# Optimization experiments

Measured on AMD Instinct MI355X. Metric: run time of the kernel, lower is better.

## Reference

```python
import jax, jax.numpy as jnp
import numpy as np

N, E = 50000, 1600000
IN_DIM, EMBED, OUT = 512, 128, 64


def setup_inputs() -> dict:
    key = jax.random.key(0)
    k = jax.random.split(key, 8)
    x = jax.random.normal(k[0], (N, IN_DIM), dtype=jnp.float32)
    edge_index = jax.random.randint(k[1], (2, E), 0, N, dtype=jnp.int32)
    W_dense = jax.random.normal(k[2], (EMBED, IN_DIM), dtype=jnp.float32) * 0.02
    b_dense = jnp.zeros((EMBED,), dtype=jnp.float32)
    W_gat = jax.random.normal(k[3], (OUT, EMBED), dtype=jnp.float32) * 0.05
    att_src = jax.random.normal(k[4], (OUT,), dtype=jnp.float32) * 0.1
    att_dst = jax.random.normal(k[5], (OUT,), dtype=jnp.float32) * 0.1
    b_gat = jnp.zeros((OUT,), dtype=jnp.float32)
    return {"x": x, "edge_index": edge_index, "W_dense": W_dense, "b_dense": b_dense,
            "W_gat": W_gat, "att_src": att_src, "att_dst": att_dst, "b_gat": b_gat}


def reference(x, edge_index, W_dense, b_dense, W_gat, att_src, att_dst, b_gat):
    # dense -> LeakyReLU(0.01) (nn.LeakyReLU default)
    h = jax.nn.leaky_relu(x @ W_dense.T + b_dense, negative_slope=0.01)  # [N, EMBED]
    n = h.shape[0]
    # GATConv (PyG, heads=1, add_self_loops=True, negative_slope=0.2)
    loops = jnp.arange(n, dtype=edge_index.dtype)
    src = jnp.concatenate([edge_index[0], loops])
    dst = jnp.concatenate([edge_index[1], loops])
    g = h @ W_gat.T  # [N, OUT]
    a_src = g @ att_src  # [N]
    a_dst = g @ att_dst  # [N]
    e = jax.nn.leaky_relu(a_src[src] + a_dst[dst], negative_slope=0.2)  # [E+N]
    # segment softmax over destination neighborhoods (self loops guarantee non-empty)
    m = jax.ops.segment_max(e, dst, num_segments=n)
    e = jnp.exp(e - m[dst])
    denom = jax.ops.segment_sum(e, dst, num_segments=n)
    alpha = e / denom[dst]
    out = jax.ops.segment_sum(g[src] * alpha[:, None], dst, num_segments=n) + b_gat
    # original returns ([embed_x], [embed_x]); we return the single embedding tensor
    return out
```

## Files before the change

kernel.cpp:

```cpp
#include <hip/hip_runtime.h>
#include <math.h>

#define IN_DIM 512
#define EMBED 128
#define OUT_DIM 64

typedef __attribute__((ext_vector_type(8))) short bf16x8;
typedef __attribute__((ext_vector_type(4))) float f32x4;

__device__ __forceinline__ float lrelu(float v, float s) { return v > 0.f ? v : v * s; }

__device__ __forceinline__ float readlane_f(float v, int l) {
  return __int_as_float(__builtin_amdgcn_readlane(__float_as_int(v), l));
}

__device__ __forceinline__ unsigned short f2bf(float f) {
  unsigned int u = __float_as_uint(f);
  u += 0x7fff + ((u >> 16) & 1);
  return (unsigned short)(u >> 16);
}
__device__ __forceinline__ float bf2f(unsigned short h) {
  return __uint_as_float(((unsigned int)h) << 16);
}

#define LDA 40

__global__ __launch_bounds__(256) void gemm1_mfma_kernel(
    const float* __restrict__ x, const float* __restrict__ Wd,
    const float* __restrict__ bd, float* __restrict__ h, int N) {
  __shared__ __align__(16) unsigned short Ah[128][LDA];
  __shared__ __align__(16) unsigned short Al[128][LDA];
  __shared__ __align__(16) unsigned short Bh[64][LDA];
  __shared__ __align__(16) unsigned short Bl[64][LDA];

  const int tid = threadIdx.x;
  const int lane = tid & 63;
  const int wid = tid >> 6;
  const int wr = wid >> 1, wc = wid & 1;
  const int mblk = blockIdx.x * 128;
  const int nblk = blockIdx.y * 64;
  const int quad = lane >> 4;
  const int l15 = lane & 15;

  const int arow = tid >> 1, acb = (tid & 1) * 16;
  const int brow = tid >> 2, bcb = (tid & 3) * 8;
  const bool avalid = (mblk + arow) < N;
  const float* aptr = x + (size_t)(mblk + arow) * IN_DIM + acb;
  const float* bptr = Wd + (size_t)(nblk + brow) * IN_DIM + bcb;

  f32x4 acc[4][2];
#pragma unroll
  for (int i = 0; i < 4; ++i)
#pragma unroll
    for (int j = 0; j < 2; ++j) acc[i][j] = (f32x4){0.f, 0.f, 0.f, 0.f};

  for (int k0 = 0; k0 < IN_DIM; k0 += 32) {
    float4 t0, t1, t2, t3;
    if (avalid) {
      t0 = *(const float4*)(aptr + k0);
      t1 = *(const float4*)(aptr + k0 + 4);
      t2 = *(const float4*)(aptr + k0 + 8);
      t3 = *(const float4*)(aptr + k0 + 12);
    } else {
      t0 = t1 = t2 = t3 = make_float4(0.f, 0.f, 0.f, 0.f);
    }
    float4 u0 = *(const float4*)(bptr + k0);
    float4 u1 = *(const float4*)(bptr + k0 + 4);

    float av[16] = {t0.x, t0.y, t0.z, t0.w, t1.x, t1.y, t1.z, t1.w,
                    t2.x, t2.y, t2.z, t2.w, t3.x, t3.y, t3.z, t3.w};
    union { unsigned short us[16]; uint4 v[2]; } AH, AL;
#pragma unroll
    for (int i = 0; i < 16; ++i) {
      unsigned short hi = f2bf(av[i]);
      AH.us[i] = hi;
      AL.us[i] = f2bf(av[i] - bf2f(hi));
    }
    float bv[8] = {u0.x, u0.y, u0.z, u0.w, u1.x, u1.y, u1.z, u1.w};
    union { unsigned short us[8]; uint4 v; } BH, BL;
#pragma unroll
    for (int i = 0; i < 8; ++i) {
      unsigned short hi = f2bf(bv[i]);
      BH.us[i] = hi;
      BL.us[i] = f2bf(bv[i] - bf2f(hi));
    }

    __syncthreads();
    *(uint4*)&Ah[arow][acb] = AH.v[0];
    *(uint4*)&Ah[arow][acb + 8] = AH.v[1];
    *(uint4*)&Al[arow][acb] = AL.v[0];
    *(uint4*)&Al[arow][acb + 8] = AL.v[1];
    *(uint4*)&Bh[brow][bcb] = BH.v;
    *(uint4*)&Bl[brow][bcb] = BL.v;
    __syncthreads();

    bf16x8 ah[4], al[4], bh[2], bl[2];
#pragma unroll
    for (int mi = 0; mi < 4; ++mi) {
      int r = wr * 64 + mi * 16 + l15;
      ah[mi] = *(const bf16x8*)&Ah[r][quad * 8];
      al[mi] = *(const bf16x8*)&Al[r][quad * 8];
    }
#pragma unroll
    for (int ni = 0; ni < 2; ++ni) {
      int r = wc * 32 + ni * 16 + l15;
      bh[ni] = *(const bf16x8*)&Bh[r][quad * 8];
      bl[ni] = *(const bf16x8*)&Bl[r][quad * 8];
    }
#pragma unroll
    for (int mi = 0; mi < 4; ++mi)
#pragma unroll
      for (int ni = 0; ni < 2; ++ni) {
        acc[mi][ni] = __builtin_amdgcn_mfma_f32_16x16x32_bf16(ah[mi], bh[ni], acc[mi][ni], 0, 0, 0);
        acc[mi][ni] = __builtin_amdgcn_mfma_f32_16x16x32_bf16(al[mi], bh[ni], acc[mi][ni], 0, 0, 0);
        acc[mi][ni] = __builtin_amdgcn_mfma_f32_16x16x32_bf16(ah[mi], bl[ni], acc[mi][ni], 0, 0, 0);
      }
  }

#pragma unroll
  for (int mi = 0; mi < 4; ++mi)
#pragma unroll
    for (int ni = 0; ni < 2; ++ni) {
      int n = nblk + wc * 32 + ni * 16 + l15;
      float b = bd[n];
#pragma unroll
      for (int r = 0; r < 4; ++r) {
        int m = mblk + wr * 64 + mi * 16 + quad * 4 + r;
        if (m < N) h[(size_t)m * EMBED + n] = lrelu(acc[mi][ni][r] + b, 0.01f);
      }
    }
}

__global__ __launch_bounds__(256) void gemm2_mfma_kernel(
    const float* __restrict__ h, const float* __restrict__ Wg,
    const float* __restrict__ att_src, const float* __restrict__ att_dst,
    float* __restrict__ g, float* __restrict__ a_src, float* __restrict__ a_dst,
    int N) {
  __shared__ __align__(16) unsigned short Ah[128][LDA];
  __shared__ __align__(16) unsigned short Al[128][LDA];
  __shared__ __align__(16) unsigned short Bh[64][LDA];
  __shared__ __align__(16) unsigned short Bl[64][LDA];

  const int tid = threadIdx.x;
  const int lane = tid & 63;
  const int wid = tid >> 6;
  const int wr = wid >> 1, wc = wid & 1;
  const int mblk = blockIdx.x * 128;
  const int quad = lane >> 4;
  const int l15 = lane & 15;

  const int arow = tid >> 1, acb = (tid & 1) * 16;
  const int brow = tid >> 2, bcb = (tid & 3) * 8;
  const bool avalid = (mblk + arow) < N;
  const float* aptr = h + (size_t)(mblk + arow) * EMBED + acb;
  const float* bptr = Wg + (size_t)brow * EMBED + bcb;

  f32x4 acc[4][2];
#pragma unroll
  for (int i = 0; i < 4; ++i)
#pragma unroll
    for (int j = 0; j < 2; ++j) acc[i][j] = (f32x4){0.f, 0.f, 0.f, 0.f};

  for (int k0 = 0; k0 < EMBED; k0 += 32) {
    float4 t0, t1, t2, t3;
    if (avalid) {
      t0 = *(const float4*)(aptr + k0);
      t1 = *(const float4*)(aptr + k0 + 4);
      t2 = *(const float4*)(aptr + k0 + 8);
      t3 = *(const float4*)(aptr + k0 + 12);
    } else {
      t0 = t1 = t2 = t3 = make_float4(0.f, 0.f, 0.f, 0.f);
    }
    float4 u0 = *(const float4*)(bptr + k0);
    float4 u1 = *(const float4*)(bptr + k0 + 4);

    float av[16] = {t0.x, t0.y, t0.z, t0.w, t1.x, t1.y, t1.z, t1.w,
                    t2.x, t2.y, t2.z, t2.w, t3.x, t3.y, t3.z, t3.w};
    union { unsigned short us[16]; uint4 v[2]; } AH, AL;
#pragma unroll
    for (int i = 0; i < 16; ++i) {
      unsigned short hi = f2bf(av[i]);
      AH.us[i] = hi;
      AL.us[i] = f2bf(av[i] - bf2f(hi));
    }
    float bv[8] = {u0.x, u0.y, u0.z, u0.w, u1.x, u1.y, u1.z, u1.w};
    union { unsigned short us[8]; uint4 v; } BH, BL;
#pragma unroll
    for (int i = 0; i < 8; ++i) {
      unsigned short hi = f2bf(bv[i]);
      BH.us[i] = hi;
      BL.us[i] = f2bf(bv[i] - bf2f(hi));
    }

    __syncthreads();
    *(uint4*)&Ah[arow][acb] = AH.v[0];
    *(uint4*)&Ah[arow][acb + 8] = AH.v[1];
    *(uint4*)&Al[arow][acb] = AL.v[0];
    *(uint4*)&Al[arow][acb + 8] = AL.v[1];
    *(uint4*)&Bh[brow][bcb] = BH.v;
    *(uint4*)&Bl[brow][bcb] = BL.v;
    __syncthreads();

    bf16x8 ah[4], al[4], bh[2], bl[2];
#pragma unroll
    for (int mi = 0; mi < 4; ++mi) {
      int r = wr * 64 + mi * 16 + l15;
      ah[mi] = *(const bf16x8*)&Ah[r][quad * 8];
      al[mi] = *(const bf16x8*)&Al[r][quad * 8];
    }
#pragma unroll
    for (int ni = 0; ni < 2; ++ni) {
      int r = wc * 32 + ni * 16 + l15;
      bh[ni] = *(const bf16x8*)&Bh[r][quad * 8];
      bl[ni] = *(const bf16x8*)&Bl[r][quad * 8];
    }
#pragma unroll
    for (int mi = 0; mi < 4; ++mi)
#pragma unroll
      for (int ni = 0; ni < 2; ++ni) {
        acc[mi][ni] = __builtin_amdgcn_mfma_f32_16x16x32_bf16(ah[mi], bh[ni], acc[mi][ni], 0, 0, 0);
        acc[mi][ni] = __builtin_amdgcn_mfma_f32_16x16x32_bf16(al[mi], bh[ni], acc[mi][ni], 0, 0, 0);
        acc[mi][ni] = __builtin_amdgcn_mfma_f32_16x16x32_bf16(ah[mi], bl[ni], acc[mi][ni], 0, 0, 0);
      }
  }

  float as_[2], ad_[2];
#pragma unroll
  for (int ni = 0; ni < 2; ++ni) {
    int n = wc * 32 + ni * 16 + l15;
    as_[ni] = att_src[n];
    ad_[ni] = att_dst[n];
  }
#pragma unroll
  for (int mi = 0; mi < 4; ++mi) {
#pragma unroll
    for (int r = 0; r < 4; ++r) {
      int m = mblk + wr * 64 + mi * 16 + quad * 4 + r;
      float ps = acc[mi][0][r] * as_[0] + acc[mi][1][r] * as_[1];
      float pd = acc[mi][0][r] * ad_[0] + acc[mi][1][r] * ad_[1];
#pragma unroll
      for (int d = 1; d < 16; d <<= 1) {
        ps += __shfl_xor(ps, d, 64);
        pd += __shfl_xor(pd, d, 64);
      }
      if (m < N) {
#pragma unroll
        for (int ni = 0; ni < 2; ++ni) {
          int n = wc * 32 + ni * 16 + l15;
          g[(size_t)m * OUT_DIM + n] = acc[mi][ni][r];
        }
        if (l15 == 0 && wc == 0) {
          a_src[m] = ps;
          a_dst[m] = pd;
        }
      }
    }
  }
  __syncthreads();
#pragma unroll
  for (int mi = 0; mi < 4; ++mi) {
#pragma unroll
    for (int r = 0; r < 4; ++r) {
      int m = mblk + wr * 64 + mi * 16 + quad * 4 + r;
      float ps = acc[mi][0][r] * as_[0] + acc[mi][1][r] * as_[1];
      float pd = acc[mi][0][r] * ad_[0] + acc[mi][1][r] * ad_[1];
#pragma unroll
      for (int d = 1; d < 16; d <<= 1) {
        ps += __shfl_xor(ps, d, 64);
        pd += __shfl_xor(pd, d, 64);
      }
      if (m < N && l15 == 0 && wc == 1) {
        atomicAdd(&a_src[m], ps);
        atomicAdd(&a_dst[m], pd);
      }
    }
  }
}

__global__ void zero_kernel(int* __restrict__ p, int n) {
  int i = blockIdx.x * blockDim.x + threadIdx.x;
  if (i < n) p[i] = 0;
}

__global__ void scatter_pad_kernel(const int* __restrict__ ei,
                                   const float* __restrict__ a_src,
                                   const float* __restrict__ a_dst,
                                   int* __restrict__ next,
                                   int2* __restrict__ stage, int E, int N,
                                   int CAP) {
  int i = blockIdx.x * blockDim.x + threadIdx.x;
  if (i < E + N) {
    int s, d;
    if (i < E) {
      s = ei[i];
      d = ei[E + i];
    } else {
      s = d = i - E;
    }
    float e = a_src[s] + a_dst[d];
    e = e > 0.f ? e : 0.2f * e;
    int pos = atomicAdd(&next[d], 1);
    if (pos < CAP) {
      int2 rec;
      rec.x = s;
      rec.y = __float_as_int(e);
      stage[(size_t)d * CAP + pos] = rec;
    }
  }
}

__global__ __launch_bounds__(256) void aggregate_kernel(
    const int* __restrict__ next, const int2* __restrict__ stage,
    const float* __restrict__ g, const float* __restrict__ b_gat,
    float* __restrict__ out, int N, int CAP) {
  const int lane = threadIdx.x & 63;
  const int node = blockIdx.x * 4 + (threadIdx.x >> 6);
  if (node >= N) return;
  const int cnt_n = min(next[node], CAP);
  const int2* rowp = stage + (size_t)node * CAP;

  float m = -1e30f;
  for (int j = lane; j < cnt_n; j += 64)
    m = fmaxf(m, __int_as_float(rowp[j].y));
#pragma unroll
  for (int d = 1; d < 64; d <<= 1) m = fmaxf(m, __shfl_xor(m, d, 64));

  float l = 0.f;
  for (int j = lane; j < cnt_n; j += 64)
    l += __expf(__int_as_float(rowp[j].y) - m);
#pragma unroll
  for (int d = 1; d < 64; d <<= 1) l += __shfl_xor(l, d, 64);
  const float inv_l = 1.f / l;

  float acc0 = 0.f, acc1 = 0.f, acc2 = 0.f, acc3 = 0.f;
  for (int jb = 0; jb < cnt_n; jb += 64) {
    int j = jb + lane;
    float p = 0.f;
    int s = 0;
    if (j < cnt_n) {
      int2 rec = rowp[j];
      p = __expf(__int_as_float(rec.y) - m) * inv_l;
      s = rec.x;
    }
    const int cnt = min(64, cnt_n - jb);
    int jj = 0;
    for (; jj + 4 <= cnt; jj += 4) {
      int s0 = __builtin_amdgcn_readlane(s, jj);
      int s1 = __builtin_amdgcn_readlane(s, jj + 1);
      int s2 = __builtin_amdgcn_readlane(s, jj + 2);
      int s3 = __builtin_amdgcn_readlane(s, jj + 3);
      float p0 = readlane_f(p, jj);
      float p1 = readlane_f(p, jj + 1);
      float p2 = readlane_f(p, jj + 2);
      float p3 = readlane_f(p, jj + 3);
      acc0 += p0 * g[((size_t)s0 << 6) + lane];
      acc1 += p1 * g[((size_t)s1 << 6) + lane];
      acc2 += p2 * g[((size_t)s2 << 6) + lane];
      acc3 += p3 * g[((size_t)s3 << 6) + lane];
    }
    for (; jj < cnt; ++jj) {
      int s0 = __builtin_amdgcn_readlane(s, jj);
      float p0 = readlane_f(p, jj);
      acc0 += p0 * g[((size_t)s0 << 6) + lane];
    }
  }
  out[(size_t)node * OUT_DIM + lane] = (acc0 + acc1) + (acc2 + acc3) + b_gat[lane];
}

extern "C" void kernel_launch(void* const* d_in, const int* in_sizes, int n_in,
                              void* d_out, int out_size, void* d_ws, size_t ws_size,
                              hipStream_t stream) {
  const float* x = (const float*)d_in[0];
  const int* ei = (const int*)d_in[1];
  const float* Wd = (const float*)d_in[2];
  const float* bd = (const float*)d_in[3];
  const float* Wg = (const float*)d_in[4];
  const float* att_src = (const float*)d_in[5];
  const float* att_dst = (const float*)d_in[6];
  const float* bg = (const float*)d_in[7];
  float* out = (float*)d_out;

  const int N = in_sizes[0] / IN_DIM;
  const int E = in_sizes[1] / 2;
  const int T = E + N;

  char* ws = (char*)d_ws;
  size_t off = 0;
  auto alloc = [&](size_t bytes) -> void* {
    void* p = ws + off;
    off += (bytes + 15) & ~(size_t)15;
    return p;
  };
  float* h = (float*)alloc((size_t)N * EMBED * 4);
  float* g = (float*)alloc((size_t)N * OUT_DIM * 4);
  float* a_src = (float*)alloc((size_t)N * 4);
  float* a_dst = (float*)alloc((size_t)N * 4);
  int* next = (int*)alloc((size_t)N * 4);
  size_t rem = (ws_size > off + 256) ? (ws_size - off - 256) : 0;
  int CAP = (int)(rem / ((size_t)N * 8));
  if (CAP > 80) CAP = 80;
  int2* stage = (int2*)alloc((size_t)N * CAP * 8);

  hipLaunchKernelGGL(gemm1_mfma_kernel, dim3((N + 127) / 128, 2), dim3(256), 0,
                     stream, x, Wd, bd, h, N);
  hipLaunchKernelGGL(gemm2_mfma_kernel, dim3((N + 127) / 128), dim3(256), 0,
                     stream, h, Wg, att_src, att_dst, g, a_src, a_dst, N);
  hipLaunchKernelGGL(zero_kernel, dim3((N + 255) / 256), dim3(256), 0, stream,
                     next, N);
  hipLaunchKernelGGL(scatter_pad_kernel, dim3((T + 255) / 256), dim3(256), 0,
                     stream, ei, a_src, a_dst, next, stage, E, N, CAP);
  hipLaunchKernelGGL(aggregate_kernel, dim3((N + 3) / 4), dim3(256), 0, stream,
                     next, stage, g, bg, out, N, CAP);
}
```

Before: 343.1 us.

## Split scatter cursors into per-block-group buckets and defer attention logits

```diff
diff --git a/kernel.cpp b/kernel.cpp
--- a/kernel.cpp
+++ b/kernel.cpp
@@ -4,6 +4,7 @@
 #define IN_DIM 512
 #define EMBED 128
 #define OUT_DIM 64
+#define NGRP 8
 
 typedef __attribute__((ext_vector_type(8))) short bf16x8;
 typedef __attribute__((ext_vector_type(4))) float f32x4;
@@ -282,12 +283,11 @@
   if (i < n) p[i] = 0;
 }
 
-__global__ void scatter_pad_kernel(const int* __restrict__ ei,
-                                   const float* __restrict__ a_src,
-                                   const float* __restrict__ a_dst,
-                                   int* __restrict__ next,
-                                   int2* __restrict__ stage, int E, int N,
-                                   int CAP) {
+__global__ void scatter4_kernel(const int* __restrict__ ei,
+                                int* __restrict__ cursor,
+                                int* __restrict__ stage, int E, int N,
+                                int CAP_X) {
+  const int grp = blockIdx.x & (NGRP - 1);
   int i = blockIdx.x * blockDim.x + threadIdx.x;
   if (i < E + N) {
     int s, d;
@@ -297,52 +297,66 @@
     } else {
       s = d = i - E;
     }
-    float e = a_src[s] + a_dst[d];
-    e = e > 0.f ? e : 0.2f * e;
-    int pos = atomicAdd(&next[d], 1);
-    if (pos < CAP) {
-      int2 rec;
-      rec.x = s;
-      rec.y = __float_as_int(e);
-      stage[(size_t)d * CAP + pos] = rec;
-    }
+    int pos = atomicAdd(&cursor[(size_t)grp * N + d], 1);
+    if (pos < CAP_X) stage[((size_t)grp * N + d) * CAP_X + pos] = s;
   }
 }
 
 __global__ __launch_bounds__(256) void aggregate_kernel(
-    const int* __restrict__ next, const int2* __restrict__ stage,
+    const int* __restrict__ cursor, const int* __restrict__ stage,
+    const float* __restrict__ a_src, const float* __restrict__ a_dst,
     const float* __restrict__ g, const float* __restrict__ b_gat,
-    float* __restrict__ out, int N, int CAP) {
+    float* __restrict__ out, int N, int CAP_X) {
   const int lane = threadIdx.x & 63;
   const int node = blockIdx.x * 4 + (threadIdx.x >> 6);
   if (node >= N) return;
-  const int cnt_n = min(next[node], CAP);
-  const int2* rowp = stage + (size_t)node * CAP;
-
-  float m = -1e30f;
-  for (int j = lane; j < cnt_n; j += 64)
-    m = fmaxf(m, __int_as_float(rowp[j].y));
+
+  int pre[NGRP];
+  int run = 0;
+#pragma unroll
+  for (int xk = 0; xk < NGRP; ++xk) {
+    pre[xk] = run;
+    run += min(cursor[(size_t)xk * N + node], CAP_X);
+  }
+  const int total = min(run, 128);
+  const float adn = a_dst[node];
+
+  int s_r[2];
+  float e_r[2];
+#pragma unroll
+  for (int c = 0; c < 2; ++c) {
+    int j = c * 64 + lane;
+    int off = 0, xs = 0;
+#pragma unroll
+    for (int k = 1; k < NGRP; ++k)
+      if (j >= pre[k]) { xs = k; off = pre[k]; }
+    if (j < total) {
+      int s = stage[((size_t)xs * N + node) * CAP_X + (j - off)];
+      float e = a_src[s] + adn;
+      s_r[c] = s;
+      e_r[c] = e > 0.f ? e : 0.2f * e;
+    } else {
+      s_r[c] = 0;
+      e_r[c] = -1e30f;
+    }
+  }
+
+  float m = fmaxf(e_r[0], e_r[1]);
 #pragma unroll
   for (int d = 1; d < 64; d <<= 1) m = fmaxf(m, __shfl_xor(m, d, 64));
 
-  float l = 0.f;
-  for (int j = lane; j < cnt_n; j += 64)
-    l += __expf(__int_as_float(rowp[j].y) - m);
+  float l = __expf(e_r[0] - m) + __expf(e_r[1] - m);
 #pragma unroll
   for (int d = 1; d < 64; d <<= 1) l += __shfl_xor(l, d, 64);
   const float inv_l = 1.f / l;
 
   float acc0 = 0.f, acc1 = 0.f, acc2 = 0.f, acc3 = 0.f;
-  for (int jb = 0; jb < cnt_n; jb += 64) {
-    int j = jb + lane;
-    float p = 0.f;
-    int s = 0;
-    if (j < cnt_n) {
-      int2 rec = rowp[j];
-      p = __expf(__int_as_float(rec.y) - m) * inv_l;
-      s = rec.x;
-    }
-    const int cnt = min(64, cnt_n - jb);
+#pragma unroll
+  for (int c = 0; c < 2; ++c) {
+    const int cnt = min(64, total - c * 64);
+    if (cnt <= 0) break;
+    float p = __expf(e_r[c] - m) * inv_l;
+    int s = s_r[c];
     int jj = 0;
     for (; jj + 4 <= cnt; jj += 4) {
       int s0 = __builtin_amdgcn_readlane(s, jj);
@@ -395,20 +409,20 @@
   float* g = (float*)alloc((size_t)N * OUT_DIM * 4);
   float* a_src = (float*)alloc((size_t)N * 4);
   float* a_dst = (float*)alloc((size_t)N * 4);
-  int* next = (int*)alloc((size_t)N * 4);
+  int* cursor = (int*)alloc((size_t)N * NGRP * 4);
   size_t rem = (ws_size > off + 256) ? (ws_size - off - 256) : 0;
-  int CAP = (int)(rem / ((size_t)N * 8));
-  if (CAP > 80) CAP = 80;
-  int2* stage = (int2*)alloc((size_t)N * CAP * 8);
+  int CAP_X = (int)(rem / ((size_t)N * NGRP * 4));
+  if (CAP_X > 20) CAP_X = 20;
+  int* stage = (int*)alloc((size_t)N * NGRP * CAP_X * 4);
 
   hipLaunchKernelGGL(gemm1_mfma_kernel, dim3((N + 127) / 128, 2), dim3(256), 0,
                      stream, x, Wd, bd, h, N);
   hipLaunchKernelGGL(gemm2_mfma_kernel, dim3((N + 127) / 128), dim3(256), 0,
                      stream, h, Wg, att_src, att_dst, g, a_src, a_dst, N);
-  hipLaunchKernelGGL(zero_kernel, dim3((N + 255) / 256), dim3(256), 0, stream,
-                     next, N);
-  hipLaunchKernelGGL(scatter_pad_kernel, dim3((T + 255) / 256), dim3(256), 0,
-                     stream, ei, a_src, a_dst, next, stage, E, N, CAP);
+  hipLaunchKernelGGL(zero_kernel, dim3((N * NGRP + 255) / 256), dim3(256), 0,
+                     stream, cursor, N * NGRP);
+  hipLaunchKernelGGL(scatter4_kernel, dim3((T + 255) / 256), dim3(256), 0,
+                     stream, ei, cursor, stage, E, N, CAP_X);
   hipLaunchKernelGGL(aggregate_kernel, dim3((N + 3) / 4), dim3(256), 0, stream,
-                     next, stage, g, bg, out, N, CAP);
-}
+                     cursor, stage, a_src, a_dst, g, bg, out, N, CAP_X);
+}
```

Measured after the change: 381.9 us. 1.11x slower.

## Replace capped padded per-node staging with two-pass bucketed CSR build

Applied to the files above, without the earlier changes.

```diff
diff --git a/kernel.cpp b/kernel.cpp
--- a/kernel.cpp
+++ b/kernel.cpp
@@ -4,6 +4,9 @@
 #define IN_DIM 512
 #define EMBED 128
 #define OUT_DIM 64
+#define NBPAD 256
+#define SEGSH 12
+#define CAP_LDS 10240
 
 typedef __attribute__((ext_vector_type(8))) short bf16x8;
 typedef __attribute__((ext_vector_type(4))) float f32x4;
@@ -277,72 +280,168 @@
   }
 }
 
-__global__ void zero_kernel(int* __restrict__ p, int n) {
-  int i = blockIdx.x * blockDim.x + threadIdx.x;
-  if (i < n) p[i] = 0;
-}
-
-__global__ void scatter_pad_kernel(const int* __restrict__ ei,
-                                   const float* __restrict__ a_src,
-                                   const float* __restrict__ a_dst,
-                                   int* __restrict__ next,
-                                   int2* __restrict__ stage, int E, int N,
-                                   int CAP) {
-  int i = blockIdx.x * blockDim.x + threadIdx.x;
-  if (i < E + N) {
-    int s, d;
-    if (i < E) {
-      s = ei[i];
-      d = ei[E + i];
-    } else {
-      s = d = i - E;
-    }
-    float e = a_src[s] + a_dst[d];
+__global__ __launch_bounds__(256) void hist_count_kernel(
+    const int* __restrict__ ei, int* __restrict__ hist, int E, int N) {
+  __shared__ int cnt[NBPAD];
+  const int t = threadIdx.x;
+  cnt[t] = 0;
+  __syncthreads();
+  const int T = E + N;
+  const int base = blockIdx.x << SEGSH;
+#pragma unroll
+  for (int q = 0; q < (1 << SEGSH) / 256; ++q) {
+    int i = base + q * 256 + t;
+    if (i < T) {
+      int d = (i < E) ? ei[E + i] : (i - E);
+      atomicAdd(&cnt[d >> 8], 1);
+    }
+  }
+  __syncthreads();
+  hist[blockIdx.x * NBPAD + t] = cnt[t];
+}
+
+__global__ __launch_bounds__(256) void alloc_scan_kernel(
+    int* __restrict__ hist, int* __restrict__ bucket_base,
+    int* __restrict__ bucket_tot, int* __restrict__ offsets, int nblkP,
+    int NB, int N, int T) {
+  __shared__ int sc[256];
+  const int t = threadIdx.x;
+  int tot = 0;
+  for (int k = 0; k < nblkP; ++k) tot += hist[k * NBPAD + t];
+  sc[t] = tot;
+  __syncthreads();
+  for (int dlt = 1; dlt < 256; dlt <<= 1) {
+    int add = (t >= dlt) ? sc[t - dlt] : 0;
+    __syncthreads();
+    sc[t] += add;
+    __syncthreads();
+  }
+  const int bb = sc[t] - tot;
+  if (t < NB) {
+    bucket_base[t] = bb;
+    bucket_tot[t] = tot;
+  }
+  if (t == 0) offsets[N] = T;
+  int run = bb;
+  for (int k = 0; k < nblkP; ++k) {
+    int c = hist[k * NBPAD + t];
+    hist[k * NBPAD + t] = run;
+    run += c;
+  }
+}
+
+__global__ __launch_bounds__(256) void bin_kernel(
+    const int* __restrict__ ei, const int* __restrict__ hist,
+    int* __restrict__ stageB, int E, int N) {
+  __shared__ int cnt[NBPAD];
+  __shared__ int basev[NBPAD];
+  const int t = threadIdx.x;
+  cnt[t] = 0;
+  basev[t] = hist[blockIdx.x * NBPAD + t];
+  __syncthreads();
+  const int T = E + N;
+  const int base = blockIdx.x << SEGSH;
+#pragma unroll
+  for (int q = 0; q < (1 << SEGSH) / 256; ++q) {
+    int i = base + q * 256 + t;
+    if (i < T) {
+      int s, d;
+      if (i < E) {
+        s = ei[i];
+        d = ei[E + i];
+      } else {
+        s = d = i - E;
+      }
+      int b = d >> 8;
+      int r = atomicAdd(&cnt[b], 1);
+      stageB[basev[b] + r] = (s << 8) | (d & 255);
+    }
+  }
+}
+
+__global__ __launch_bounds__(256) void build_kernel(
+    const int* __restrict__ stageB, const int* __restrict__ bucket_base,
+    const int* __restrict__ bucket_tot, const float* __restrict__ a_src,
+    const float* __restrict__ a_dst, int* __restrict__ offsets,
+    int2* __restrict__ csr_pack, int N) {
+  __shared__ int cnt[256];
+  __shared__ int pre[256];
+  __shared__ int cur[256];
+  __shared__ int2 buf[CAP_LDS];
+  const int b = blockIdx.x;
+  const int t = threadIdx.x;
+  const int base = bucket_base[b];
+  const int tot = bucket_tot[b];
+  cnt[t] = 0;
+  __syncthreads();
+  const int* sp = stageB + base;
+  for (int i = t; i < tot; i += 256) atomicAdd(&cnt[sp[i] & 255], 1);
+  __syncthreads();
+  int v = cnt[t];
+  pre[t] = v;
+  __syncthreads();
+  for (int dlt = 1; dlt < 256; dlt <<= 1) {
+    int add = (t >= dlt) ? pre[t - dlt] : 0;
+    __syncthreads();
+    pre[t] += add;
+    __syncthreads();
+  }
+  const int excl = pre[t] - v;
+  cur[t] = excl;
+  const int d_self = (b << 8) | t;
+  if (d_self < N) offsets[d_self] = base + excl;
+  __syncthreads();
+  for (int i = t; i < tot; i += 256) {
+    int rec = sp[i];
+    int dl = rec & 255;
+    int s = rec >> 8;
+    float e = a_src[s] + a_dst[(b << 8) | dl];
     e = e > 0.f ? e : 0.2f * e;
-    int pos = atomicAdd(&next[d], 1);
-    if (pos < CAP) {
-      int2 rec;
-      rec.x = s;
-      rec.y = __float_as_int(e);
-      stage[(size_t)d * CAP + pos] = rec;
-    }
-  }
+    int pos = atomicAdd(&cur[dl], 1);
+    int2 r2 = make_int2(s, __float_as_int(e));
+    if (pos < CAP_LDS)
+      buf[pos] = r2;
+    else
+      csr_pack[base + pos] = r2;
+  }
+  __syncthreads();
+  const int lim = min(tot, CAP_LDS);
+  for (int i = t; i < lim; i += 256) csr_pack[base + i] = buf[i];
 }
 
 __global__ __launch_bounds__(256) void aggregate_kernel(
-    const int* __restrict__ next, const int2* __restrict__ stage,
+    const int* __restrict__ offsets, const int2* __restrict__ csr_pack,
     const float* __restrict__ g, const float* __restrict__ b_gat,
-    float* __restrict__ out, int N, int CAP) {
+    float* __restrict__ out, int N) {
   const int lane = threadIdx.x & 63;
   const int node = blockIdx.x * 4 + (threadIdx.x >> 6);
   if (node >= N) return;
-  const int cnt_n = min(next[node], CAP);
-  const int2* rowp = stage + (size_t)node * CAP;
+  const int beg = offsets[node], end = offsets[node + 1];
 
   float m = -1e30f;
-  for (int j = lane; j < cnt_n; j += 64)
-    m = fmaxf(m, __int_as_float(rowp[j].y));
+  for (int j = beg + lane; j < end; j += 64)
+    m = fmaxf(m, __int_as_float(csr_pack[j].y));
 #pragma unroll
   for (int d = 1; d < 64; d <<= 1) m = fmaxf(m, __shfl_xor(m, d, 64));
 
   float l = 0.f;
-  for (int j = lane; j < cnt_n; j += 64)
-    l += __expf(__int_as_float(rowp[j].y) - m);
+  for (int j = beg + lane; j < end; j += 64)
+    l += __expf(__int_as_float(csr_pack[j].y) - m);
 #pragma unroll
   for (int d = 1; d < 64; d <<= 1) l += __shfl_xor(l, d, 64);
   const float inv_l = 1.f / l;
 
   float acc0 = 0.f, acc1 = 0.f, acc2 = 0.f, acc3 = 0.f;
-  for (int jb = 0; jb < cnt_n; jb += 64) {
+  for (int jb = beg; jb < end; jb += 64) {
     int j = jb + lane;
     float p = 0.f;
     int s = 0;
-    if (j < cnt_n) {
-      int2 rec = rowp[j];
+    if (j < end) {
+      int2 rec = csr_pack[j];
       p = __expf(__int_as_float(rec.y) - m) * inv_l;
       s = rec.x;
     }
-    const int cnt = min(64, cnt_n - jb);
+    const int cnt = min(64, end - jb);
     int jj = 0;
     for (; jj + 4 <= cnt; jj += 4) {
       int s0 = __builtin_amdgcn_readlane(s, jj);
@@ -383,6 +482,8 @@
   const int N = in_sizes[0] / IN_DIM;
   const int E = in_sizes[1] / 2;
   const int T = E + N;
+  const int NB = (N + 255) >> 8;
+  const int nblkP = (T + (1 << SEGSH) - 1) >> SEGSH;
 
   char* ws = (char*)d_ws;
   size_t off = 0;
@@ -395,20 +496,26 @@
   float* g = (float*)alloc((size_t)N * OUT_DIM * 4);
   float* a_src = (float*)alloc((size_t)N * 4);
   float* a_dst = (float*)alloc((size_t)N * 4);
-  int* next = (int*)alloc((size_t)N * 4);
-  size_t rem = (ws_size > off + 256) ? (ws_size - off - 256) : 0;
-  int CAP = (int)(rem / ((size_t)N * 8));
-  if (CAP > 80) CAP = 80;
-  int2* stage = (int2*)alloc((size_t)N * CAP * 8);
+  int* offsets = (int*)alloc((size_t)(N + 1) * 4);
+  int* hist = (int*)alloc((size_t)nblkP * NBPAD * 4);
+  int* bucket_base = (int*)alloc((size_t)NBPAD * 4);
+  int* bucket_tot = (int*)alloc((size_t)NBPAD * 4);
+  int* stageB = (int*)alloc((size_t)T * 4);
+  int2* csr_pack = (int2*)alloc((size_t)T * 8);
 
   hipLaunchKernelGGL(gemm1_mfma_kernel, dim3((N + 127) / 128, 2), dim3(256), 0,
                      stream, x, Wd, bd, h, N);
   hipLaunchKernelGGL(gemm2_mfma_kernel, dim3((N + 127) / 128), dim3(256), 0,
                      stream, h, Wg, att_src, att_dst, g, a_src, a_dst, N);
-  hipLaunchKernelGGL(zero_kernel, dim3((N + 255) / 256), dim3(256), 0, stream,
-                     next, N);
-  hipLaunchKernelGGL(scatter_pad_kernel, dim3((T + 255) / 256), dim3(256), 0,
-                     stream, ei, a_src, a_dst, next, stage, E, N, CAP);
+  hipLaunchKernelGGL(hist_count_kernel, dim3(nblkP), dim3(256), 0, stream,
+                     ei, hist, E, N);
+  hipLaunchKernelGGL(alloc_scan_kernel, dim3(1), dim3(256), 0, stream,
+                     hist, bucket_base, bucket_tot, offsets, nblkP, NB, N, T);
+  hipLaunchKernelGGL(bin_kernel, dim3(nblkP), dim3(256), 0, stream,
+                     ei, hist, stageB, E, N);
+  hipLaunchKernelGGL(build_kernel, dim3(NB), dim3(256), 0, stream,
+                     stageB, bucket_base, bucket_tot, a_src, a_dst, offsets,
+                     csr_pack, N);
   hipLaunchKernelGGL(aggregate_kernel, dim3((N + 3) / 4), dim3(256), 0, stream,
-                     next, stage, g, bg, out, N, CAP);
-}
+                     offsets, csr_pack, g, bg, out, N);
+}
```

Result: slower. 406.6 us (+18.5%).
